# Performance work log

Hardware: AMD Instinct MI355X
Metric: run time of the kernel (lower is better)

The kernel has to match this reference:

```python
import jax, jax.numpy as jnp
import numpy as np

B = 8192
BASE = 340            # base_state_size (one frame)
STACK = 4             # frame stack -> state_size = 1360
SLOT_F = 4            # [present, dx, dy, dist] per slot
CAT_DEFS = [16, 8, 4, 4, 4, 8, 8, 8, 8]   # slots per category (sum = 68)
NUM_CATS = len(CAT_DEFS)
CAT_INFO = []
_off = 59
for _slots in CAT_DEFS:
    CAT_INFO.append((_off, _slots))
    _off += 1 + _slots * SLOT_F
STATE_SIZE = BASE * STACK
ATTN_DIM, HEADS = 128, 4
HEAD_DIM = ATTN_DIM // HEADS
TRUNK_H = 1024
ATOMS = 51
ACTIONS = 81
TRUNK_IN = STATE_SIZE + ATTN_DIM
NEG_INF = -1e9


def _layernorm(x, g, b, eps=1e-5):
    m = x.mean(-1, keepdims=True)
    v = ((x - m) ** 2).mean(-1, keepdims=True)
    return (x - m) * jax.lax.rsqrt(v + eps) * g + b


def setup_inputs() -> dict:
    key = jax.random.key(0)
    ks = iter(jax.random.split(key, 32))
    def w(shape, s=0.02):
        return jax.random.normal(next(ks), shape, jnp.float32) * s
    return {
        "state": jax.random.normal(next(ks), (B, STATE_SIZE), jnp.float32),
        "embed_W": w((7, ATTN_DIM)), "embed_b": jnp.zeros((ATTN_DIM,), jnp.float32),
        "ln_g": jnp.ones((ATTN_DIM,), jnp.float32), "ln_b": jnp.zeros((ATTN_DIM,), jnp.float32),
        "cls_tok": jnp.zeros((1, 1, ATTN_DIM), jnp.float32),
        "in_proj_W": w((3 * ATTN_DIM, ATTN_DIM)), "in_proj_b": jnp.zeros((3 * ATTN_DIM,), jnp.float32),
        "out_proj_W": w((ATTN_DIM, ATTN_DIM)), "out_proj_b": jnp.zeros((ATTN_DIM,), jnp.float32),
        "t0_W": w((TRUNK_IN, TRUNK_H)), "t0_b": jnp.zeros((TRUNK_H,), jnp.float32),
        "t0_g": jnp.ones((TRUNK_H,), jnp.float32), "t0_beta": jnp.zeros((TRUNK_H,), jnp.float32),
        "t1_W": w((TRUNK_H, TRUNK_H)), "t1_b": jnp.zeros((TRUNK_H,), jnp.float32),
        "t1_g": jnp.ones((TRUNK_H,), jnp.float32), "t1_beta": jnp.zeros((TRUNK_H,), jnp.float32),
        "val_fc_W": w((TRUNK_H, TRUNK_H // 2)), "val_fc_b": jnp.zeros((TRUNK_H // 2,), jnp.float32),
        "val_out_W": w((TRUNK_H // 2, ATOMS)), "val_out_b": jnp.zeros((ATOMS,), jnp.float32),
        "adv_fc_W": w((TRUNK_H, TRUNK_H // 2)), "adv_fc_b": jnp.zeros((TRUNK_H // 2,), jnp.float32),
        "adv_out_W": w((TRUNK_H // 2, ACTIONS * ATOMS)), "adv_out_b": jnp.zeros((ACTIONS * ATOMS,), jnp.float32),
    }


def _build_tokens(state):
    """Per-category gather + delta + pack -> (B, 68, 7) tokens and (B, 68) empty-mask."""
    b = state.shape[0]
    latest_off = (STACK - 1) * BASE
    prev_off = (STACK - 2) * BASE
    toks, masks = [], []
    for cat_id, (base, slots) in enumerate(CAT_INFO):
        lo = latest_off + base + 1
        po = prev_off + base + 1
        latest = state[:, lo:lo + slots * SLOT_F].reshape(b, slots, SLOT_F)
        prev = state[:, po:po + slots * SLOT_F].reshape(b, slots, SLOT_F)
        present = latest[:, :, 0]
        dx, dy, dist = latest[:, :, 1:2], latest[:, :, 2:3], latest[:, :, 3:4]
        vel_valid = ((present > 0.5) & (prev[:, :, 0] > 0.5))[:, :, None].astype(state.dtype)
        ddx = (dx - prev[:, :, 1:2]) * vel_valid
        ddy = (dy - prev[:, :, 2:3]) * vel_valid
        cat_norm = jnp.full((b, slots, 1), cat_id / (NUM_CATS - 1), state.dtype)
        toks.append(jnp.concatenate([dx, dy, dist, ddx, ddy, cat_norm, present[:, :, None]], axis=2))
        masks.append(present < 0.5)
    tokens = jnp.concatenate(toks, axis=1)
    mask = jnp.concatenate(masks, axis=1)          # True = slot empty
    all_empty = jnp.all(mask, axis=1, keepdims=True)
    mask = mask & ~all_empty                       # if everything empty, unmask all
    return tokens, mask


def reference(state, embed_W, embed_b, ln_g, ln_b, cls_tok, in_proj_W, in_proj_b,
              out_proj_W, out_proj_b, t0_W, t0_b, t0_g, t0_beta, t1_W, t1_b, t1_g, t1_beta,
              val_fc_W, val_fc_b, val_out_W, val_out_b, adv_fc_W, adv_fc_b, adv_out_W, adv_out_b):
    b = state.shape[0]
    tokens, mask = _build_tokens(state)
    x = _layernorm(tokens @ embed_W + embed_b, ln_g, ln_b)
    x = jnp.concatenate([jnp.broadcast_to(cls_tok, (b, 1, ATTN_DIM)), x], axis=1)  # (B, S+1, E)
    kpm = jnp.concatenate([jnp.zeros((b, 1), bool), mask], axis=1)                  # (B, S+1)
    qkv = x @ in_proj_W.T + in_proj_b
    q, k, v = jnp.split(qkv, 3, axis=-1)
    def to_heads(t):
        return t.reshape(b, -1, HEADS, HEAD_DIM).transpose(0, 2, 1, 3)
    q, k, v = to_heads(q), to_heads(k), to_heads(v)
    scores = jnp.einsum('bhqd,bhkd->bhqk', q, k) / np.float32(np.sqrt(HEAD_DIM))
    scores = jnp.where(kpm[:, None, None, :], NEG_INF, scores)
    attn = jax.nn.softmax(scores, axis=-1)
    out = jnp.einsum('bhqk,bhkd->bhqd', attn, v).transpose(0, 2, 1, 3).reshape(b, -1, ATTN_DIM)
    out = out @ out_proj_W.T + out_proj_b
    pooled = out[:, 0, :]                           # CLS pooling
    h = jnp.concatenate([state, pooled], axis=1)
    h = jax.nn.relu(_layernorm(h @ t0_W + t0_b, t0_g, t0_beta))
    h = jax.nn.relu(_layernorm(h @ t1_W + t1_b, t1_g, t1_beta))
    val = jax.nn.relu(h @ val_fc_W + val_fc_b)
    val = (val @ val_out_W + val_out_b).reshape(b, 1, ATOMS)
    adv = jax.nn.relu(h @ adv_fc_W + adv_fc_b)
    adv = (adv @ adv_out_W + adv_out_b).reshape(b, ACTIONS, ATOMS)
    q_atoms = val + adv - adv.mean(axis=1, keepdims=True)
    return jax.nn.softmax(q_atoms, axis=2)          # (B, 81, 51) C51 probabilities
```

## Files before the change

### kernel.cpp

```cpp
#include <hip/hip_runtime.h>

typedef unsigned short u16;
typedef unsigned int u32;
typedef __attribute__((ext_vector_type(4))) unsigned int u32x4;
typedef __attribute__((ext_vector_type(8))) __bf16 bf16x8;
typedef __attribute__((ext_vector_type(4))) float f32x4;

#define MFMA(a, b, c) __builtin_amdgcn_mfma_f32_16x16x32_bf16(a, b, c, 0, 0, 0)

__device__ __forceinline__ float b2f(u16 h) {
    union { unsigned int u; float f; } v; v.u = ((unsigned int)h) << 16; return v.f;
}
__device__ __forceinline__ u16 f2b(float f) {
    union { float f; unsigned int u; } v; v.f = f;
    unsigned int r = v.u + 0x7fffu + ((v.u >> 16) & 1u);
    return (u16)(r >> 16);
}
__device__ __forceinline__ float gread(const void* p, size_t i, int isf32) {
    return isf32 ? ((const float*)p)[i] : b2f(((const u16*)p)[i]);
}

__global__ __launch_bounds__(256) void detect_kernel(const void* __restrict__ state,
                                                     int* __restrict__ flag)
{
    __shared__ int cnt;
    if (threadIdx.x == 0) cnt = 0;
    __syncthreads();
    const u16* p = (const u16*)state;
    int local = 0;
    for (int i = threadIdx.x; i < 4096; i += 256) {
        int e = (p[i] >> 7) & 0xFF;
        if (e >= 200) local++;
    }
    atomicAdd(&cnt, local);
    __syncthreads();
    if (threadIdx.x == 0) *flag = (cnt >= 32) ? 1 : 0;
}

__global__ __launch_bounds__(256) void norm_small_kernel(
    const void* __restrict__ embW, const void* __restrict__ embB,
    const void* __restrict__ lng,  const void* __restrict__ lnb,
    const void* __restrict__ cls,  const void* __restrict__ ipW,
    const void* __restrict__ ipb,  const void* __restrict__ opW,
    const void* __restrict__ opb,  const void* __restrict__ t0g,
    const void* __restrict__ t0be, const void* __restrict__ t1g,
    const void* __restrict__ t1be, u16* __restrict__ dst,
    const int* __restrict__ flagp)
{
    int idx = blockIdx.x * 256 + threadIdx.x;
    if (idx >= 71552) return;
    int isf32 = *flagp;
    const void* src; int rel;
    if      (idx < 896)   { src = embW; rel = idx; }
    else if (idx < 1024)  { src = embB; rel = idx - 896; }
    else if (idx < 1152)  { src = lng;  rel = idx - 1024; }
    else if (idx < 1280)  { src = lnb;  rel = idx - 1152; }
    else if (idx < 1408)  { src = cls;  rel = idx - 1280; }
    else if (idx < 50560) { src = ipW;  rel = idx - 1408; }
    else if (idx < 50944) { src = ipb;  rel = idx - 50560; }
    else if (idx < 67328) { src = opW;  rel = idx - 50944; }
    else if (idx < 67456) { src = opb;  rel = idx - 67328; }
    else if (idx < 68480) { src = t0g;  rel = idx - 67456; }
    else if (idx < 69504) { src = t0be; rel = idx - 68480; }
    else if (idx < 70528) { src = t1g;  rel = idx - 69504; }
    else                  { src = t1be; rel = idx - 70528; }
    dst[idx] = isf32 ? f2b(((const float*)src)[rel]) : ((const u16*)src)[rel];
}

__global__ __launch_bounds__(256) void pack_kernel(
    const void* __restrict__ t0W, const void* __restrict__ t1W,
    const void* __restrict__ vfW, const void* __restrict__ afW,
    const void* __restrict__ voW, const void* __restrict__ aoW,
    const void* __restrict__ t0b, const void* __restrict__ t1b,
    const void* __restrict__ vfb, const void* __restrict__ afb,
    const void* __restrict__ vob, const void* __restrict__ aob,
    const int* __restrict__ flagp,
    u16* __restrict__ Bt0, u16* __restrict__ Bt1, u16* __restrict__ Btfc,
    u16* __restrict__ Btao, u16* __restrict__ Btvo,
    float* __restrict__ bias0, float* __restrict__ bias1, float* __restrict__ biasfc,
    float* __restrict__ biasao, float* __restrict__ biasvo)
{
    int idx = blockIdx.x * 256 + threadIdx.x;
    const int isf32 = *flagp;
    if (idx < 1540096) {
        int n = idx / 1504, k = idx % 1504;
        Bt0[idx] = (k < 1488) ? f2b(gread(t0W, (size_t)k * 1024 + n, isf32)) : (u16)0;
        return;
    }
    idx -= 1540096;
    if (idx < 1048576) {
        int n = idx >> 10, k = idx & 1023;
        Bt1[idx] = f2b(gread(t1W, (size_t)k * 1024 + n, isf32));
        return;
    }
    idx -= 1048576;
    if (idx < 1048576) {
        int n = idx >> 10, k = idx & 1023;
        Btfc[idx] = (n < 512) ? f2b(gread(vfW, (size_t)k * 512 + n, isf32))
                              : f2b(gread(afW, (size_t)k * 512 + (n - 512), isf32));
        return;
    }
    idx -= 1048576;
    if (idx < 2162688) {
        int n = idx / 512, k = idx & 511;
        Btao[idx] = (n < 4131) ? f2b(gread(aoW, (size_t)k * 4131 + n, isf32)) : (u16)0;
        return;
    }
    idx -= 2162688;
    if (idx < 65536) {
        int n = idx >> 9, k = idx & 511;
        Btvo[idx] = (n < 51) ? f2b(gread(voW, (size_t)k * 51 + n, isf32)) : (u16)0;
        return;
    }
    idx -= 65536;
    if (idx < 1024) { bias0[idx] = gread(t0b, idx, isf32); return; }
    idx -= 1024;
    if (idx < 1024) { bias1[idx] = gread(t1b, idx, isf32); return; }
    idx -= 1024;
    if (idx < 1024) { biasfc[idx] = (idx < 512) ? gread(vfb, idx, isf32)
                                                : gread(afb, idx - 512, isf32); return; }
    idx -= 1024;
    if (idx < 4224) { biasao[idx] = (idx < 4131) ? gread(aob, idx, isf32) : 0.f; return; }
    idx -= 4224;
    if (idx < 128)  { biasvo[idx] = (idx < 51) ? gread(vob, idx, isf32) : 0.f; return; }
}

__global__ __launch_bounds__(384) void prep_cls_kernel(
    const u16* __restrict__ cls, const u16* __restrict__ ipW, const u16* __restrict__ ipb,
    float* __restrict__ qvec, float* __restrict__ vcls, float* __restrict__ s0)
{
    __shared__ float qkv[384];
    int tid = threadIdx.x;
    float a = b2f(ipb[tid]);
    for (int c = 0; c < 128; c++) a += b2f(ipW[(size_t)tid * 128 + c]) * b2f(cls[c]);
    qkv[tid] = a;
    __syncthreads();
    if (tid < 128) { qvec[tid] = qkv[tid]; vcls[tid] = qkv[256 + tid]; }
    if (tid < 4) {
        float s = 0.f;
        for (int d = 0; d < 32; d++) s += qkv[tid * 32 + d] * qkv[128 + tid * 32 + d];
        s0[tid] = s * 0.17677669529663687f;
    }
}

__global__ __launch_bounds__(256) void prep2_kernel(
    const u16* __restrict__ ipW, const u16* __restrict__ ipb,
    const float* __restrict__ qvec, float* __restrict__ rmat, float* __restrict__ cb)
{
    int tid = threadIdx.x;
    for (int j = 0; j < 2; j++) {
        int idx = j * 256 + tid;
        int h = idx >> 7, c = idx & 127;
        float acc = 0.f;
        for (int k = 0; k < 32; k++)
            acc += qvec[32 * h + k] * b2f(ipW[(size_t)(128 + 32 * h + k) * 128 + c]);
        rmat[idx] = acc;
    }
    if (tid < 4) {
        float acc = 0.f;
        for (int k = 0; k < 32; k++)
            acc += qvec[32 * tid + k] * b2f(ipb[128 + 32 * tid + k]);
        cb[tid] = acc;
    }
}

__global__ __launch_bounds__(256) void attn_kernel(
    const void* __restrict__ state, const int* __restrict__ flagp,
    const u16* __restrict__ embW, const u16* __restrict__ embB,
    const u16* __restrict__ lng, const u16* __restrict__ lnb,
    const u16* __restrict__ ipW, const u16* __restrict__ ipb,
    const u16* __restrict__ opW, const u16* __restrict__ opb,
    const float* __restrict__ vcls, const float* __restrict__ s0,
    const float* __restrict__ rmat, const float* __restrict__ cb,
    u16* __restrict__ A0)
{
    __shared__ __align__(16) u16 Xs[68][136];
    __shared__ float embWs[896];
    __shared__ float embBs[128], lngs[128], lnbs[128];
    __shared__ float rs[4][132];
    __shared__ float cbs[4];
    __shared__ float tok[68][8];
    __shared__ float maskf[68];
    __shared__ int   cnt;
    __shared__ float sc[68][4];
    __shared__ float pp[72][4];
    __shared__ float zs[4][132];
    __shared__ float yv[128];

    const int b   = blockIdx.x;
    const int tid = threadIdx.x;
    const int wave = tid >> 6, lane = tid & 63;
    const int isf32 = *flagp;
    u16* arow = A0 + (size_t)b * 1504;

    for (int i = tid; i < 896; i += 256) embWs[i] = b2f(embW[i]);
    if (tid < 128) { embBs[tid] = b2f(embB[tid]); lngs[tid] = b2f(lng[tid]); lnbs[tid] = b2f(lnb[tid]); }
    for (int i = tid; i < 512; i += 256) rs[i >> 7][i & 127] = rmat[i];
    if (tid < 4) cbs[tid] = cb[tid];
    if (tid == 0) cnt = 0;

    if (isf32) {
        const float* srowf = (const float*)state + (size_t)b * 1360;
        for (int i = tid; i < 170; i += 256) {
            union { u16 h[8]; u32x4 v; } u;
            #pragma unroll
            for (int j = 0; j < 8; j++) u.h[j] = f2b(srowf[i * 8 + j]);
            *(u32x4*)&arow[i * 8] = u.v;
        }
    } else {
        const u16* srow = (const u16*)state + (size_t)b * 1360;
        for (int i = tid; i < 170; i += 256)
            *(u32x4*)&arow[i * 8] = *(const u32x4*)&srow[i * 8];
    }
    if (tid < 16) arow[1488 + tid] = 0;
    __syncthreads();

    if (tid < 68) {
        const int cum[10]    = {0, 16, 24, 28, 32, 36, 44, 52, 60, 68};
        const int basetab[9] = {59, 124, 157, 174, 191, 208, 241, 274, 307};
        int t = tid, cat = 0;
        while (t >= cum[cat + 1]) cat++;
        int slot = t - cum[cat];
        int off  = basetab[cat] + 1 + slot * 4;
        auto SR = [&](int idx) -> float {
            return isf32 ? ((const float*)state)[(size_t)b * 1360 + idx]
                         : b2f(((const u16*)state)[(size_t)b * 1360 + idx]);
        };
        float lp    = SR(1020 + off + 0);
        float ldx   = SR(1020 + off + 1);
        float ldy   = SR(1020 + off + 2);
        float ldist = SR(1020 + off + 3);
        float ppres = SR(680 + off + 0);
        float pdx   = SR(680 + off + 1);
        float pdy   = SR(680 + off + 2);
        float vv = (lp > 0.5f && ppres > 0.5f) ? 1.f : 0.f;
        tok[t][0] = ldx; tok[t][1] = ldy; tok[t][2] = ldist;
        tok[t][3] = (ldx - pdx) * vv; tok[t][4] = (ldy - pdy) * vv;
        tok[t][5] = (float)cat * 0.125f; tok[t][6] = lp;
        int m = (lp < 0.5f) ? 1 : 0;
        maskf[t] = (float)m;
        if (m) atomicAdd(&cnt, 1);
    }
    __syncthreads();
    const bool all_empty = (cnt == 68);

    for (int t = wave; t < 68; t += 4) {
        float e0 = embBs[lane], e1 = embBs[lane + 64];
        #pragma unroll
        for (int f = 0; f < 7; f++) {
            float tv = tok[t][f];
            e0 += tv * embWs[f * 128 + lane];
            e1 += tv * embWs[f * 128 + lane + 64];
        }
        float s = e0 + e1;
        #pragma unroll
        for (int m = 1; m < 64; m <<= 1) s += __shfl_xor(s, m);
        float mean = s * (1.f / 128.f);
        float d0 = e0 - mean, d1 = e1 - mean;
        float v = d0 * d0 + d1 * d1;
        #pragma unroll
        for (int m = 1; m < 64; m <<= 1) v += __shfl_xor(v, m);
        float inv = rsqrtf(v * (1.f / 128.f) + 1e-5f);
        Xs[t][lane]      = f2b(d0 * inv * lngs[lane]      + lnbs[lane]);
        Xs[t][lane + 64] = f2b(d1 * inv * lngs[lane + 64] + lnbs[lane + 64]);
    }
    __syncthreads();

    for (int it = 0; it < 2; it++) {
        int idx = it * 256 + tid;
        if (idx < 272) {
            int t = idx >> 2, h = idx & 3;
            float acc = cbs[h];
            const u32* xrow = (const u32*)&Xs[t][0];
            #pragma unroll 4
            for (int c = 0; c < 64; c++) {
                u32 w = xrow[c];
                union { u32 u; float f; } lo, hi;
                lo.u = w << 16; hi.u = w & 0xffff0000u;
                acc += lo.f * rs[h][2 * c] + hi.f * rs[h][2 * c + 1];
            }
            float s = acc * 0.17677669529663687f;
            if (maskf[t] > 0.5f && !all_empty) s = -1e9f;
            sc[t][h] = s;
        }
    }
    __syncthreads();

    {
        int h = wave;
        float v0 = (lane == 0) ? s0[h] : sc[lane - 1][h];
        float v1 = (lane <= 4) ? sc[lane + 63][h] : -1e30f;
        float m = fmaxf(v0, v1);
        #pragma unroll
        for (int mm = 1; mm < 64; mm <<= 1) m = fmaxf(m, __shfl_xor(m, mm));
        float e0 = __expf(v0 - m);
        float e1 = (lane <= 4) ? __expf(v1 - m) : 0.f;
        float sum = e0 + e1;
        #pragma unroll
        for (int mm = 1; mm < 64; mm <<= 1) sum += __shfl_xor(sum, mm);
        float rinv = 1.f / sum;
        pp[lane][h] = e0 * rinv;
        if (lane <= 4) pp[lane + 64][h] = e1 * rinv;
    }
    __syncthreads();

    for (int j = 0; j < 2; j++) {
        int idx = j * 256 + tid;
        int h = idx >> 7, c = idx & 127;
        float acc = 0.f;
        for (int t = 0; t < 68; t++) acc += pp[t + 1][h] * b2f(Xs[t][c]);
        zs[h][c] = acc;
    }
    __syncthreads();

    {
        int d = tid >> 1, half = tid & 1, h = d >> 5;
        float acc = 0.f;
        const u16* wrow = ipW + (size_t)(256 + d) * 128 + 64 * half;
        const float* zrow = &zs[h][64 * half];
        #pragma unroll
        for (int j = 0; j < 8; j++) {
            bf16x8 w = *(const bf16x8*)(wrow + j * 8);
            #pragma unroll
            for (int k = 0; k < 8; k++) acc += (float)w[k] * zrow[j * 8 + k];
        }
        float other = __shfl_xor(acc, 1);
        if (half == 0) {
            float p0 = pp[0][h];
            yv[d] = acc + other + p0 * vcls[d] + (1.f - p0) * b2f(ipb[256 + d]);
        }
    }
    __syncthreads();

    {
        int e = tid >> 1, half = tid & 1;
        float acc = 0.f;
        const u16* wrow = opW + (size_t)e * 128 + 64 * half;
        const float* yrow = &yv[64 * half];
        #pragma unroll
        for (int j = 0; j < 8; j++) {
            bf16x8 w = *(const bf16x8*)(wrow + j * 8);
            #pragma unroll
            for (int k = 0; k < 8; k++) acc += (float)w[k] * yrow[j * 8 + k];
        }
        float other = __shfl_xor(acc, 1);
        if (half == 0) arow[1360 + e] = f2b(acc + other + b2f(opb[e]));
    }
}

#define LDSP 40
template <int EPI>
__global__ __launch_bounds__(256) void gemm_bt(
    const u16* __restrict__ A, int lda, const u16* __restrict__ Bt, int ldb,
    const float* __restrict__ bias, void* __restrict__ Cout, int ldc, int K)
{
    __shared__ __align__(16) u16 As[128 * LDSP];
    __shared__ __align__(16) u16 Bs[128 * LDSP];
    const int tid = threadIdx.x;
    const int row0 = blockIdx.y * 128, col0 = blockIdx.x * 128;
    const int wave = tid >> 6, lane = tid & 63;
    const int wm = wave >> 1, wn = wave & 1;
    const int lr = lane & 15, lq = lane >> 4;

    f32x4 acc[4][4] = {};

    for (int k0 = 0; k0 < K; k0 += 32) {
        __syncthreads();
        #pragma unroll
        for (int c = tid; c < 512; c += 256) {
            int r = c >> 2, q = c & 3;
            *(u32x4*)&As[r * LDSP + q * 8] = *(const u32x4*)&A[(size_t)(row0 + r) * lda + k0 + q * 8];
            *(u32x4*)&Bs[r * LDSP + q * 8] = *(const u32x4*)&Bt[(size_t)(col0 + r) * ldb + k0 + q * 8];
        }
        __syncthreads();
        bf16x8 af[4], bf[4];
        #pragma unroll
        for (int i = 0; i < 4; i++) af[i] = *(const bf16x8*)&As[(wm * 64 + i * 16 + lr) * LDSP + lq * 8];
        #pragma unroll
        for (int j = 0; j < 4; j++) bf[j] = *(const bf16x8*)&Bs[(wn * 64 + j * 16 + lr) * LDSP + lq * 8];
        #pragma unroll
        for (int i = 0; i < 4; i++)
            #pragma unroll
            for (int j = 0; j < 4; j++)
                acc[i][j] = MFMA(af[i], bf[j], acc[i][j]);
    }

    const int cbase = col0 + wn * 64;
    const int rbase = row0 + wm * 64;
    float bv[4];
    #pragma unroll
    for (int j = 0; j < 4; j++) bv[j] = bias[cbase + j * 16 + lr];
    #pragma unroll
    for (int i = 0; i < 4; i++) {
        #pragma unroll
        for (int j = 0; j < 4; j++) {
            int cc = cbase + j * 16 + lr;
            #pragma unroll
            for (int r = 0; r < 4; r++) {
                int rr = rbase + i * 16 + lq * 4 + r;
                float v = acc[i][j][r] + bv[j];
                if (EPI == 1) v = fmaxf(v, 0.f);
                if (EPI == 0) ((float*)Cout)[(size_t)rr * ldc + cc] = v;
                else          ((u16*)Cout)[(size_t)rr * ldc + cc] = f2b(v);
            }
        }
    }
}

__global__ __launch_bounds__(256) void ln_relu_kernel(
    const float* __restrict__ C, const u16* __restrict__ g, const u16* __restrict__ be,
    u16* __restrict__ H)
{
    __shared__ float red[8];
    const int b = blockIdx.x, tid = threadIdx.x;
    const float* row = C + (size_t)b * 1024;
    float x0 = row[tid], x1 = row[tid + 256], x2 = row[tid + 512], x3 = row[tid + 768];
    float s = x0 + x1 + x2 + x3;
    #pragma unroll
    for (int m = 1; m < 64; m <<= 1) s += __shfl_xor(s, m);
    if ((tid & 63) == 0) red[tid >> 6] = s;
    __syncthreads();
    float mean = (red[0] + red[1] + red[2] + red[3]) * (1.f / 1024.f);
    float d0 = x0 - mean, d1 = x1 - mean, d2 = x2 - mean, d3 = x3 - mean;
    float v = d0 * d0 + d1 * d1 + d2 * d2 + d3 * d3;
    #pragma unroll
    for (int m = 1; m < 64; m <<= 1) v += __shfl_xor(v, m);
    if ((tid & 63) == 0) red[4 + (tid >> 6)] = v;
    __syncthreads();
    float inv = rsqrtf((red[4] + red[5] + red[6] + red[7]) * (1.f / 1024.f) + 1e-5f);
    u16* hrow = H + (size_t)b * 1024;
    float dd[4] = {d0, d1, d2, d3};
    #pragma unroll
    for (int i = 0; i < 4; i++) {
        int c = tid + i * 256;
        float h = dd[i] * inv * b2f(g[c]) + b2f(be[c]);
        hrow[c] = f2b(fmaxf(h, 0.f));
    }
}

__global__ __launch_bounds__(256) void final_kernel(
    const u16* __restrict__ ADV, const u16* __restrict__ VAL,
    void* __restrict__ out, const int* __restrict__ flagp)
{
    __shared__ __align__(16) u16 advr[4136];
    __shared__ float meanv[51];
    __shared__ float valv[51];
    const int b = blockIdx.x, tid = threadIdx.x;
    const int isf32 = *flagp;
    const u16* arow = ADV + (size_t)b * 4224;
    for (int i = tid; i < 517; i += 256)
        *(u32x4*)&advr[i * 8] = *(const u32x4*)&arow[i * 8];
    if (tid < 51) valv[tid] = b2f(VAL[(size_t)b * 128 + tid]);
    __syncthreads();
    if (tid < 51) {
        float s = 0.f;
        for (int j = 0; j < 81; j++) s += b2f(advr[j * 51 + tid]);
        meanv[tid] = s * (1.f / 81.f);
    }
    __syncthreads();
    const int wave = tid >> 6, lane = tid & 63;
    for (int a = wave; a < 81; a += 4) {
        float q = (lane < 51) ? valv[lane] + b2f(advr[a * 51 + lane]) - meanv[lane] : -1e30f;
        float m = q;
        #pragma unroll
        for (int mm = 1; mm < 64; mm <<= 1) m = fmaxf(m, __shfl_xor(m, mm));
        float e = (lane < 51) ? __expf(q - m) : 0.f;
        float s = e;
        #pragma unroll
        for (int mm = 1; mm < 64; mm <<= 1) s += __shfl_xor(s, mm);
        if (lane < 51) {
            float r = e / s;
            size_t oi = (size_t)b * 4131 + a * 51 + lane;
            if (isf32) ((float*)out)[oi] = r;
            else       ((u16*)out)[oi]  = f2b(r);
        }
    }
}

extern "C" void kernel_launch(void* const* d_in, const int* in_sizes, int n_in,
                              void* d_out, int out_size, void* d_ws, size_t ws_size,
                              hipStream_t stream)
{
    (void)in_sizes; (void)n_in; (void)out_size; (void)ws_size;
    const void* state = d_in[0];
    const void* embW  = d_in[1];
    const void* embB  = d_in[2];
    const void* lng   = d_in[3];
    const void* lnb   = d_in[4];
    const void* cls   = d_in[5];
    const void* ipW   = d_in[6];
    const void* ipb   = d_in[7];
    const void* opW   = d_in[8];
    const void* opb   = d_in[9];
    const void* t0W   = d_in[10];
    const void* t0b   = d_in[11];
    const void* t0g   = d_in[12];
    const void* t0be  = d_in[13];
    const void* t1W   = d_in[14];
    const void* t1b   = d_in[15];
    const void* t1g   = d_in[16];
    const void* t1be  = d_in[17];
    const void* vfW   = d_in[18];
    const void* vfb   = d_in[19];
    const void* voW   = d_in[20];
    const void* vob   = d_in[21];
    const void* afW   = d_in[22];
    const void* afb   = d_in[23];
    const void* aoW   = d_in[24];
    const void* aob   = d_in[25];

    char* ws = (char*)d_ws;
    size_t off = 0;
    auto alloc = [&](size_t bytes) -> void* {
        off = (off + 255) & ~(size_t)255;
        void* p = ws + off;
        off += bytes;
        return p;
    };
    int*   flag   = (int*)alloc(4);
    u16*   Nbuf   = (u16*)alloc(71552 * 2);
    float* qvec   = (float*)alloc(128 * 4);
    float* vcls   = (float*)alloc(128 * 4);
    float* s0     = (float*)alloc(4 * 4);
    float* rmat   = (float*)alloc(512 * 4);
    float* cb     = (float*)alloc(4 * 4);
    float* bias0  = (float*)alloc(1024 * 4);
    float* bias1  = (float*)alloc(1024 * 4);
    float* biasfc = (float*)alloc(1024 * 4);
    float* biasao = (float*)alloc(4224 * 4);
    float* biasvo = (float*)alloc(128 * 4);
    u16* Bt0  = (u16*)alloc(1024L * 1504 * 2);
    u16* Bt1  = (u16*)alloc(1024L * 1024 * 2);
    u16* Btfc = (u16*)alloc(1024L * 1024 * 2);
    u16* Btao = (u16*)alloc(4224L * 512 * 2);
    u16* Btvo = (u16*)alloc(128L * 512 * 2);
    u16* A0   = (u16*)alloc(8192L * 1504 * 2);
    float* C0 = (float*)alloc(8192L * 1024 * 4);
    u16* H0   = (u16*)alloc(8192L * 1024 * 2);
    u16* ADV  = A0;
    u16* H1   = (u16*)alloc(8192L * 1024 * 2);
    u16* VA   = (u16*)alloc(8192L * 1024 * 2);
    u16* VAL  = (u16*)alloc(8192L * 128 * 2);

    u16* Nemb  = Nbuf + 0;
    u16* NembB = Nbuf + 896;
    u16* Nlng  = Nbuf + 1024;
    u16* Nlnb  = Nbuf + 1152;
    u16* Ncls  = Nbuf + 1280;
    u16* Nipw  = Nbuf + 1408;
    u16* Nipb  = Nbuf + 50560;
    u16* Nopw  = Nbuf + 50944;
    u16* Nopb  = Nbuf + 67328;
    u16* Nt0g  = Nbuf + 67456;
    u16* Nt0be = Nbuf + 68480;
    u16* Nt1g  = Nbuf + 69504;
    u16* Nt1be = Nbuf + 70528;

    detect_kernel<<<1, 256, 0, stream>>>(state, flag);
    norm_small_kernel<<<280, 256, 0, stream>>>(embW, embB, lng, lnb, cls, ipW, ipb,
                                               opW, opb, t0g, t0be, t1g, t1be,
                                               Nbuf, flag);
    pack_kernel<<<22941, 256, 0, stream>>>(t0W, t1W, vfW, afW, voW, aoW,
                                           t0b, t1b, vfb, afb, vob, aob, flag,
                                           Bt0, Bt1, Btfc, Btao, Btvo,
                                           bias0, bias1, biasfc, biasao, biasvo);
    prep_cls_kernel<<<1, 384, 0, stream>>>(Ncls, Nipw, Nipb, qvec, vcls, s0);
    prep2_kernel<<<1, 256, 0, stream>>>(Nipw, Nipb, qvec, rmat, cb);
    attn_kernel<<<8192, 256, 0, stream>>>(state, flag, Nemb, NembB, Nlng, Nlnb,
                                          Nipw, Nipb, Nopw, Nopb,
                                          vcls, s0, rmat, cb, A0);
    gemm_bt<0><<<dim3(8, 64), 256, 0, stream>>>(A0, 1504, Bt0, 1504, bias0, C0, 1024, 1504);
    ln_relu_kernel<<<8192, 256, 0, stream>>>(C0, Nt0g, Nt0be, H0);
    gemm_bt<0><<<dim3(8, 64), 256, 0, stream>>>(H0, 1024, Bt1, 1024, bias1, C0, 1024, 1024);
    ln_relu_kernel<<<8192, 256, 0, stream>>>(C0, Nt1g, Nt1be, H1);
    gemm_bt<1><<<dim3(8, 64), 256, 0, stream>>>(H1, 1024, Btfc, 1024, biasfc, VA, 1024, 1024);
    gemm_bt<2><<<dim3(33, 64), 256, 0, stream>>>(VA + 512, 1024, Btao, 512, biasao, ADV, 4224, 512);
    gemm_bt<2><<<dim3(1, 64), 256, 0, stream>>>(VA, 1024, Btvo, 512, biasvo, VAL, 128, 512);
    final_kernel<<<8192, 256, 0, stream>>>(ADV, VAL, d_out, flag);
}
```

Baseline: 785.6 us.

## Use direct global-to-LDS loads in GEMM, cache state row in LDS, merge value output

The GEMM tile loader now uses global_load_lds 16-byte transfers into unpadded LDS tiles, so A and B tiles no longer pass through registers. The attention kernel copies the state row into shared memory as floats for the token gather, restructures the score dot product with a k-split plus shuffle reduction, and computes two heads per thread in the weighted-sum step. The value-output weights and bias are packed next to the advantage weights so both results land in one ADV row, which removes a separate VAL buffer and the extra global read in the final kernel. Dropping the LDS padding may bring back bank conflicts on the fragment reads.

Result: faster. 745.0 us (-5.2%).

```diff
diff --git a/kernel.cpp b/kernel.cpp
--- a/kernel.cpp
+++ b/kernel.cpp
@@ -18,6 +18,11 @@
 }
 __device__ __forceinline__ float gread(const void* p, size_t i, int isf32) {
     return isf32 ? ((const float*)p)[i] : b2f(((const u16*)p)[i]);
+}
+__device__ __forceinline__ void gl_lds16(const u16* g, u16* l) {
+    __builtin_amdgcn_global_load_lds(
+        (const __attribute__((address_space(1))) void*)(g),
+        (__attribute__((address_space(3))) void*)(l), 16, 0, 0);
 }
 
 __global__ __launch_bounds__(256) void detect_kernel(const void* __restrict__ state,
@@ -76,9 +81,9 @@
     const void* __restrict__ vob, const void* __restrict__ aob,
     const int* __restrict__ flagp,
     u16* __restrict__ Bt0, u16* __restrict__ Bt1, u16* __restrict__ Btfc,
-    u16* __restrict__ Btao, u16* __restrict__ Btvo,
+    u16* __restrict__ Btao,
     float* __restrict__ bias0, float* __restrict__ bias1, float* __restrict__ biasfc,
-    float* __restrict__ biasao, float* __restrict__ biasvo)
+    float* __restrict__ biasao)
 {
     int idx = blockIdx.x * 256 + threadIdx.x;
     const int isf32 = *flagp;
@@ -101,18 +106,15 @@
         return;
     }
     idx -= 1048576;
-    if (idx < 2162688) {
+    if (idx < 2228224) {
         int n = idx / 512, k = idx & 511;
-        Btao[idx] = (n < 4131) ? f2b(gread(aoW, (size_t)k * 4131 + n, isf32)) : (u16)0;
+        u16 v = 0;
+        if (n < 4131)                  v = f2b(gread(aoW, (size_t)k * 4131 + n, isf32));
+        else if (n >= 4224 && n < 4275) v = f2b(gread(voW, (size_t)k * 51 + (n - 4224), isf32));
+        Btao[idx] = v;
         return;
     }
-    idx -= 2162688;
-    if (idx < 65536) {
-        int n = idx >> 9, k = idx & 511;
-        Btvo[idx] = (n < 51) ? f2b(gread(voW, (size_t)k * 51 + n, isf32)) : (u16)0;
-        return;
-    }
-    idx -= 65536;
+    idx -= 2228224;
     if (idx < 1024) { bias0[idx] = gread(t0b, idx, isf32); return; }
     idx -= 1024;
     if (idx < 1024) { bias1[idx] = gread(t1b, idx, isf32); return; }
@@ -120,9 +122,13 @@
     if (idx < 1024) { biasfc[idx] = (idx < 512) ? gread(vfb, idx, isf32)
                                                 : gread(afb, idx - 512, isf32); return; }
     idx -= 1024;
-    if (idx < 4224) { biasao[idx] = (idx < 4131) ? gread(aob, idx, isf32) : 0.f; return; }
-    idx -= 4224;
-    if (idx < 128)  { biasvo[idx] = (idx < 51) ? gread(vob, idx, isf32) : 0.f; return; }
+    if (idx < 4352) {
+        float v = 0.f;
+        if (idx < 4131) v = gread(aob, idx, isf32);
+        else if (idx >= 4224 && idx < 4275) v = gread(vob, idx - 4224, isf32);
+        biasao[idx] = v;
+        return;
+    }
 }
 
 __global__ __launch_bounds__(384) void prep_cls_kernel(
@@ -174,43 +180,58 @@
     const float* __restrict__ rmat, const float* __restrict__ cb,
     u16* __restrict__ A0)
 {
-    __shared__ __align__(16) u16 Xs[68][136];
-    __shared__ float embWs[896];
-    __shared__ float embBs[128], lngs[128], lnbs[128];
-    __shared__ float rs[4][132];
+    __shared__ __align__(16) u16 Xs[68][138];
+    __shared__ __align__(16) float rstk[4][33][4];
+    __shared__ __align__(16) float embWs[896];
+    __shared__ __align__(16) float tok[68][8];
+    __shared__ __align__(16) float sc[68][4];
+    __shared__ __align__(16) float pp[72][4];
+    __shared__ __align__(16) float zs[4][128];
+    __shared__ __align__(16) float yv[128];
+    __shared__ u16 embBh[128], lngh[128], lnbh[128];
+    __shared__ float maskf[68];
     __shared__ float cbs[4];
-    __shared__ float tok[68][8];
-    __shared__ float maskf[68];
     __shared__ int   cnt;
-    __shared__ float sc[68][4];
-    __shared__ float pp[72][4];
-    __shared__ float zs[4][132];
-    __shared__ float yv[128];
 
     const int b   = blockIdx.x;
     const int tid = threadIdx.x;
     const int wave = tid >> 6, lane = tid & 63;
     const int isf32 = *flagp;
     u16* arow = A0 + (size_t)b * 1504;
+    float* rowf = (float*)&Xs[0][0];
 
     for (int i = tid; i < 896; i += 256) embWs[i] = b2f(embW[i]);
-    if (tid < 128) { embBs[tid] = b2f(embB[tid]); lngs[tid] = b2f(lng[tid]); lnbs[tid] = b2f(lnb[tid]); }
-    for (int i = tid; i < 512; i += 256) rs[i >> 7][i & 127] = rmat[i];
+    if (tid < 128) { embBh[tid] = embB[tid]; lngh[tid] = lng[tid]; lnbh[tid] = lnb[tid]; }
+    for (int i = tid; i < 512; i += 256) {
+        int h = i >> 7, c = i & 127;
+        rstk[c >> 5][c & 31][h] = rmat[i];
+    }
     if (tid < 4) cbs[tid] = cb[tid];
     if (tid == 0) cnt = 0;
 
     if (isf32) {
-        const float* srowf = (const float*)state + (size_t)b * 1360;
+        const f32x4* srowf = (const f32x4*)((const float*)state + (size_t)b * 1360);
         for (int i = tid; i < 170; i += 256) {
+            f32x4 v0 = srowf[i * 2], v1 = srowf[i * 2 + 1];
             union { u16 h[8]; u32x4 v; } u;
             #pragma unroll
-            for (int j = 0; j < 8; j++) u.h[j] = f2b(srowf[i * 8 + j]);
+            for (int j = 0; j < 4; j++) { u.h[j] = f2b(v0[j]); u.h[4 + j] = f2b(v1[j]); }
             *(u32x4*)&arow[i * 8] = u.v;
+            *(f32x4*)&rowf[i * 8] = v0;
+            *(f32x4*)&rowf[i * 8 + 4] = v1;
         }
     } else {
         const u16* srow = (const u16*)state + (size_t)b * 1360;
-        for (int i = tid; i < 170; i += 256)
-            *(u32x4*)&arow[i * 8] = *(const u32x4*)&srow[i * 8];
+        for (int i = tid; i < 170; i += 256) {
+            u32x4 v = *(const u32x4*)&srow[i * 8];
+            *(u32x4*)&arow[i * 8] = v;
+            union { u32x4 v; u16 h[8]; } u; u.v = v;
+            f32x4 f0, f1;
+            #pragma unroll
+            for (int j = 0; j < 4; j++) { f0[j] = b2f(u.h[j]); f1[j] = b2f(u.h[4 + j]); }
+            *(f32x4*)&rowf[i * 8] = f0;
+            *(f32x4*)&rowf[i * 8 + 4] = f1;
+        }
     }
     if (tid < 16) arow[1488 + tid] = 0;
     __syncthreads();
@@ -222,17 +243,13 @@
         while (t >= cum[cat + 1]) cat++;
         int slot = t - cum[cat];
         int off  = basetab[cat] + 1 + slot * 4;
-        auto SR = [&](int idx) -> float {
-            return isf32 ? ((const float*)state)[(size_t)b * 1360 + idx]
-                         : b2f(((const u16*)state)[(size_t)b * 1360 + idx]);
-        };
-        float lp    = SR(1020 + off + 0);
-        float ldx   = SR(1020 + off + 1);
-        float ldy   = SR(1020 + off + 2);
-        float ldist = SR(1020 + off + 3);
-        float ppres = SR(680 + off + 0);
-        float pdx   = SR(680 + off + 1);
-        float pdy   = SR(680 + off + 2);
+        float lp    = rowf[1020 + off + 0];
+        float ldx   = rowf[1020 + off + 1];
+        float ldy   = rowf[1020 + off + 2];
+        float ldist = rowf[1020 + off + 3];
+        float ppres = rowf[680 + off + 0];
+        float pdx   = rowf[680 + off + 1];
+        float pdy   = rowf[680 + off + 2];
         float vv = (lp > 0.5f && ppres > 0.5f) ? 1.f : 0.f;
         tok[t][0] = ldx; tok[t][1] = ldy; tok[t][2] = ldist;
         tok[t][3] = (ldx - pdx) * vv; tok[t][4] = (ldy - pdy) * vv;
@@ -245,7 +262,7 @@
     const bool all_empty = (cnt == 68);
 
     for (int t = wave; t < 68; t += 4) {
-        float e0 = embBs[lane], e1 = embBs[lane + 64];
+        float e0 = b2f(embBh[lane]), e1 = b2f(embBh[lane + 64]);
         #pragma unroll
         for (int f = 0; f < 7; f++) {
             float tv = tok[t][f];
@@ -261,27 +278,37 @@
         #pragma unroll
         for (int m = 1; m < 64; m <<= 1) v += __shfl_xor(v, m);
         float inv = rsqrtf(v * (1.f / 128.f) + 1e-5f);
-        Xs[t][lane]      = f2b(d0 * inv * lngs[lane]      + lnbs[lane]);
-        Xs[t][lane + 64] = f2b(d1 * inv * lngs[lane + 64] + lnbs[lane + 64]);
+        Xs[t][lane]      = f2b(d0 * inv * b2f(lngh[lane])      + b2f(lnbh[lane]));
+        Xs[t][lane + 64] = f2b(d1 * inv * b2f(lngh[lane + 64]) + b2f(lnbh[lane + 64]));
     }
     __syncthreads();
 
     for (int it = 0; it < 2; it++) {
         int idx = it * 256 + tid;
         if (idx < 272) {
-            int t = idx >> 2, h = idx & 3;
-            float acc = cbs[h];
-            const u32* xrow = (const u32*)&Xs[t][0];
-            #pragma unroll 4
-            for (int c = 0; c < 64; c++) {
+            int t = idx >> 2, ks = idx & 3;
+            const u32* xrow = (const u32*)&Xs[t][0] + ks * 16;
+            f32x4 a = {0.f, 0.f, 0.f, 0.f};
+            #pragma unroll
+            for (int c = 0; c < 16; c++) {
                 u32 w = xrow[c];
                 union { u32 u; float f; } lo, hi;
                 lo.u = w << 16; hi.u = w & 0xffff0000u;
-                acc += lo.f * rs[h][2 * c] + hi.f * rs[h][2 * c + 1];
+                f32x4 r0 = *(const f32x4*)&rstk[ks][2 * c][0];
+                f32x4 r1 = *(const f32x4*)&rstk[ks][2 * c + 1][0];
+                a += lo.f * r0 + hi.f * r1;
             }
-            float s = acc * 0.17677669529663687f;
-            if (maskf[t] > 0.5f && !all_empty) s = -1e9f;
-            sc[t][h] = s;
+            #pragma unroll
+            for (int m = 1; m < 4; m <<= 1) {
+                a[0] += __shfl_xor(a[0], m);
+                a[1] += __shfl_xor(a[1], m);
+                a[2] += __shfl_xor(a[2], m);
+                a[3] += __shfl_xor(a[3], m);
+            }
+            float v = (ks == 0) ? a[0] : (ks == 1) ? a[1] : (ks == 2) ? a[2] : a[3];
+            float sv = (cbs[ks] + v) * 0.17677669529663687f;
+            if (maskf[t] > 0.5f && !all_empty) sv = -1e9f;
+            sc[t][ks] = sv;
         }
     }
     __syncthreads();
@@ -304,12 +331,16 @@
     }
     __syncthreads();
 
-    for (int j = 0; j < 2; j++) {
-        int idx = j * 256 + tid;
-        int h = idx >> 7, c = idx & 127;
-        float acc = 0.f;
-        for (int t = 0; t < 68; t++) acc += pp[t + 1][h] * b2f(Xs[t][c]);
-        zs[h][c] = acc;
+    {
+        int c = tid & 127, h0 = (tid >> 7) * 2;
+        float acc0 = 0.f, acc1 = 0.f;
+        #pragma unroll 4
+        for (int t = 0; t < 68; t++) {
+            float x = b2f(Xs[t][c]);
+            float2 p = *(const float2*)&pp[t + 1][h0];
+            acc0 += p.x * x; acc1 += p.y * x;
+        }
+        zs[h0][c] = acc0; zs[h0 + 1][c] = acc1;
     }
     __syncthreads();
 
@@ -348,14 +379,13 @@
     }
 }
 
-#define LDSP 40
 template <int EPI>
 __global__ __launch_bounds__(256) void gemm_bt(
     const u16* __restrict__ A, int lda, const u16* __restrict__ Bt, int ldb,
     const float* __restrict__ bias, void* __restrict__ Cout, int ldc, int K)
 {
-    __shared__ __align__(16) u16 As[128 * LDSP];
-    __shared__ __align__(16) u16 Bs[128 * LDSP];
+    __shared__ __align__(16) u16 As[128 * 32];
+    __shared__ __align__(16) u16 Bs[128 * 32];
     const int tid = threadIdx.x;
     const int row0 = blockIdx.y * 128, col0 = blockIdx.x * 128;
     const int wave = tid >> 6, lane = tid & 63;
@@ -367,17 +397,19 @@
     for (int k0 = 0; k0 < K; k0 += 32) {
         __syncthreads();
         #pragma unroll
-        for (int c = tid; c < 512; c += 256) {
-            int r = c >> 2, q = c & 3;
-            *(u32x4*)&As[r * LDSP + q * 8] = *(const u32x4*)&A[(size_t)(row0 + r) * lda + k0 + q * 8];
-            *(u32x4*)&Bs[r * LDSP + q * 8] = *(const u32x4*)&Bt[(size_t)(col0 + r) * ldb + k0 + q * 8];
+        for (int j = 0; j < 2; j++) {
+            int ci = j * 256 + wave * 64 + lane;
+            int r = ci >> 2, q = ci & 3;
+            int lbase = (j * 256 + wave * 64) * 8;
+            gl_lds16(A  + (size_t)(row0 + r) * lda + k0 + q * 8, &As[lbase]);
+            gl_lds16(Bt + (size_t)(col0 + r) * ldb + k0 + q * 8, &Bs[lbase]);
         }
         __syncthreads();
         bf16x8 af[4], bf[4];
         #pragma unroll
-        for (int i = 0; i < 4; i++) af[i] = *(const bf16x8*)&As[(wm * 64 + i * 16 + lr) * LDSP + lq * 8];
-        #pragma unroll
-        for (int j = 0; j < 4; j++) bf[j] = *(const bf16x8*)&Bs[(wn * 64 + j * 16 + lr) * LDSP + lq * 8];
+        for (int i = 0; i < 4; i++) af[i] = *(const bf16x8*)&As[(wm * 64 + i * 16 + lr) * 32 + lq * 8];
+        #pragma unroll
+        for (int j = 0; j < 4; j++) bf[j] = *(const bf16x8*)&Bs[(wn * 64 + j * 16 + lr) * 32 + lq * 8];
         #pragma unroll
         for (int i = 0; i < 4; i++)
             #pragma unroll
@@ -439,18 +471,17 @@
 }
 
 __global__ __launch_bounds__(256) void final_kernel(
-    const u16* __restrict__ ADV, const u16* __restrict__ VAL,
-    void* __restrict__ out, const int* __restrict__ flagp)
+    const u16* __restrict__ ADV, void* __restrict__ out, const int* __restrict__ flagp)
 {
     __shared__ __align__(16) u16 advr[4136];
     __shared__ float meanv[51];
     __shared__ float valv[51];
     const int b = blockIdx.x, tid = threadIdx.x;
     const int isf32 = *flagp;
-    const u16* arow = ADV + (size_t)b * 4224;
+    const u16* arow = ADV + (size_t)b * 4352;
     for (int i = tid; i < 517; i += 256)
         *(u32x4*)&advr[i * 8] = *(const u32x4*)&arow[i * 8];
-    if (tid < 51) valv[tid] = b2f(VAL[(size_t)b * 128 + tid]);
+    if (tid < 51) valv[tid] = b2f(arow[4224 + tid]);
     __syncthreads();
     if (tid < 51) {
         float s = 0.f;
@@ -527,20 +558,17 @@
     float* bias0  = (float*)alloc(1024 * 4);
     float* bias1  = (float*)alloc(1024 * 4);
     float* biasfc = (float*)alloc(1024 * 4);
-    float* biasao = (float*)alloc(4224 * 4);
-    float* biasvo = (float*)alloc(128 * 4);
+    float* biasao = (float*)alloc(4352 * 4);
     u16* Bt0  = (u16*)alloc(1024L * 1504 * 2);
     u16* Bt1  = (u16*)alloc(1024L * 1024 * 2);
     u16* Btfc = (u16*)alloc(1024L * 1024 * 2);
-    u16* Btao = (u16*)alloc(4224L * 512 * 2);
-    u16* Btvo = (u16*)alloc(128L * 512 * 2);
+    u16* Btao = (u16*)alloc(4352L * 512 * 2);
     u16* A0   = (u16*)alloc(8192L * 1504 * 2);
     float* C0 = (float*)alloc(8192L * 1024 * 4);
     u16* H0   = (u16*)alloc(8192L * 1024 * 2);
     u16* ADV  = A0;
     u16* H1   = (u16*)alloc(8192L * 1024 * 2);
     u16* VA   = (u16*)alloc(8192L * 1024 * 2);
-    u16* VAL  = (u16*)alloc(8192L * 128 * 2);
 
     u16* Nemb  = Nbuf + 0;
     u16* NembB = Nbuf + 896;
@@ -562,8 +590,8 @@
                                                Nbuf, flag);
     pack_kernel<<<22941, 256, 0, stream>>>(t0W, t1W, vfW, afW, voW, aoW,
                                            t0b, t1b, vfb, afb, vob, aob, flag,
-                                           Bt0, Bt1, Btfc, Btao, Btvo,
-                                           bias0, bias1, biasfc, biasao, biasvo);
+                                           Bt0, Bt1, Btfc, Btao,
+                                           bias0, bias1, biasfc, biasao);
     prep_cls_kernel<<<1, 384, 0, stream>>>(Ncls, Nipw, Nipb, qvec, vcls, s0);
     prep2_kernel<<<1, 256, 0, stream>>>(Nipw, Nipb, qvec, rmat, cb);
     attn_kernel<<<8192, 256, 0, stream>>>(state, flag, Nemb, NembB, Nlng, Nlnb,
@@ -574,7 +602,8 @@
     gemm_bt<0><<<dim3(8, 64), 256, 0, stream>>>(H0, 1024, Bt1, 1024, bias1, C0, 1024, 1024);
     ln_relu_kernel<<<8192, 256, 0, stream>>>(C0, Nt1g, Nt1be, H1);
     gemm_bt<1><<<dim3(8, 64), 256, 0, stream>>>(H1, 1024, Btfc, 1024, biasfc, VA, 1024, 1024);
-    gemm_bt<2><<<dim3(33, 64), 256, 0, stream>>>(VA + 512, 1024, Btao, 512, biasao, ADV, 4224, 512);
-    gemm_bt<2><<<dim3(1, 64), 256, 0, stream>>>(VA, 1024, Btvo, 512, biasvo, VAL, 128, 512);
-    final_kernel<<<8192, 256, 0, stream>>>(ADV, VAL, d_out, flag);
-}
+    gemm_bt<2><<<dim3(33, 64), 256, 0, stream>>>(VA + 512, 1024, Btao, 512, biasao, ADV, 4352, 512);
+    gemm_bt<2><<<dim3(1, 64), 256, 0, stream>>>(VA, 1024, Btao + 4224L * 512, 512,
+                                                biasao + 4224, ADV + 4224, 4352, 512);
+    final_kernel<<<8192, 256, 0, stream>>>(ADV, d_out, flag);
+}
```
